# Kernel optimization log

Measured on AMD Instinct MI355X. Metric: run time of the kernel, lower is better.

The kernel has to match this reference:

```python
import jax, jax.numpy as jnp
import numpy as np

EPS = 1e-5
DN = ('NCHW', 'OIHW', 'NCHW')


def _conv(x, w, b, stride, pad):
    y = jax.lax.conv_general_dilated(x, w, (stride, stride), [(pad, pad), (pad, pad)], dimension_numbers=DN)
    return y + b[None, :, None, None]


def _conv_t(x, w, b, stride, pad):
    # ConvTranspose2d(w: [in, out, k, k]) == conv with flipped/transposed kernel + lhs dilation
    k = w.shape[2]
    wt = jnp.flip(w, (2, 3)).transpose(1, 0, 2, 3)
    p = k - 1 - pad
    y = jax.lax.conv_general_dilated(x, wt, (1, 1), [(p, p), (p, p)], lhs_dilation=(stride, stride), dimension_numbers=DN)
    return y + b[None, :, None, None]


def _bn(x, g, b):
    # training-mode BatchNorm2d: biased batch stats over (N, H, W)
    m = x.mean((0, 2, 3), keepdims=True)
    v = x.var((0, 2, 3), keepdims=True)
    return (x - m) * jax.lax.rsqrt(v + EPS) * g[None, :, None, None] + b[None, :, None, None]


def _forward(args):
    (x, ec1_w, ec1_b, ebn1_g, ebn1_b, ec2_w, ec2_b, ebn2_g, ebn2_b,
     er1_w, er1_b, ebnr1_g, ebnr1_b, er2_w, er2_b, ebnr2_g, ebnr2_b,
     eproj_w, eproj_b, emb,
     dproj_w, dproj_b, dr1_w, dr1_b, dbn1_g, dbn1_b, dr2_w, dr2_b, dbn2_g, dbn2_b,
     dt1_w, dt1_b, dbn3_g, dbn3_b, dt2_w, dt2_b) = args
    relu = jax.nn.relu
    sg = jax.lax.stop_gradient
    # ---- encoder ----
    h = relu(_bn(_conv(x, ec1_w, ec1_b, 2, 1), ebn1_g, ebn1_b))
    h = relu(_bn(_conv(h, ec2_w, ec2_b, 2, 1), ebn2_g, ebn2_b))
    h = h + relu(_bn(_conv(h, er1_w, er1_b, 1, 1), ebnr1_g, ebnr1_b))
    h = h + relu(_bn(_conv(h, er2_w, er2_b, 1, 0), ebnr2_g, ebnr2_b))
    enc = _conv(h, eproj_w, eproj_b, 1, 0)  # [B, D, H, W]
    B, C, H, W = enc.shape
    # torch .view(B, -1, C): raw row-major reshape (no permute) -- reproduced exactly
    qi = enc.reshape(B, -1, C)  # [B, H*W, D]
    # squared euclidean distances; argmin identical to torch.cdist argmin
    d2 = (qi * qi).sum(-1, keepdims=True) - 2.0 * jnp.einsum('bnd,kd->bnk', qi, emb) + (emb * emb).sum(-1)
    closest = jnp.argmin(d2, axis=-1)  # [B, H*W]
    quantized = emb[closest]           # [B, H*W, D]
    commitment = jnp.mean((sg(quantized) - qi) ** 2)
    codebook = jnp.mean((quantized - sg(qi)) ** 2)
    quantize_loss = codebook + 0.25 * commitment
    # straight-through estimator
    quant_out = (qi + sg(quantized - qi)).reshape(B, C, H, W)
    # ---- decoder ----
    h = _conv(quant_out, dproj_w, dproj_b, 1, 0)
    h = h + relu(_bn(_conv(h, dr1_w, dr1_b, 1, 1), dbn1_g, dbn1_b))
    h = h + relu(_bn(_conv(h, dr2_w, dr2_b, 1, 1), dbn2_g, dbn2_b))
    h = relu(_bn(_conv_t(h, dt1_w, dt1_b, 2, 1), dbn3_g, dbn3_b))
    out = _conv_t(h, dt2_w, dt2_b, 2, 1)
    return out, closest, quantize_loss


def setup_inputs() -> dict:
    key = jax.random.key(0)
    ks = iter(jax.random.split(key, 32))
    def nrm(shape, fan):
        return jax.random.normal(next(ks), shape, jnp.float32) / np.float32(np.sqrt(fan))
    B, CH, S = 8, 3, 256
    K, D, HID, RES = 512, 64, 256, 128
    z = jnp.zeros
    o = jnp.ones
    return {
        'x': jax.random.normal(next(ks), (B, CH, S, S), jnp.float32),
        'ec1_w': nrm((HID, CH, 4, 4), CH * 16), 'ec1_b': z((HID,)),
        'ebn1_g': o((HID,)), 'ebn1_b': z((HID,)),
        'ec2_w': nrm((RES, HID, 4, 4), HID * 16), 'ec2_b': z((RES,)),
        'ebn2_g': o((RES,)), 'ebn2_b': z((RES,)),
        'er1_w': nrm((RES, RES, 3, 3), RES * 9), 'er1_b': z((RES,)),
        'ebnr1_g': o((RES,)), 'ebnr1_b': z((RES,)),
        'er2_w': nrm((RES, RES, 1, 1), RES), 'er2_b': z((RES,)),
        'ebnr2_g': o((RES,)), 'ebnr2_b': z((RES,)),
        'eproj_w': nrm((D, RES, 1, 1), RES), 'eproj_b': z((D,)),
        'emb': jax.random.normal(next(ks), (K, D), jnp.float32),
        'dproj_w': nrm((RES, D, 1, 1), D), 'dproj_b': z((RES,)),
        'dr1_w': nrm((RES, RES, 3, 3), RES * 9), 'dr1_b': z((RES,)),
        'dbn1_g': o((RES,)), 'dbn1_b': z((RES,)),
        'dr2_w': nrm((RES, RES, 3, 3), RES * 9), 'dr2_b': z((RES,)),
        'dbn2_g': o((RES,)), 'dbn2_b': z((RES,)),
        'dt1_w': nrm((RES, HID, 4, 4), RES * 16), 'dt1_b': z((HID,)),
        'dbn3_g': o((HID,)), 'dbn3_b': z((HID,)),
        'dt2_w': nrm((HID, CH, 4, 4), HID * 16), 'dt2_b': z((CH,)),
    }


def reference(x, ec1_w, ec1_b, ebn1_g, ebn1_b, ec2_w, ec2_b, ebn2_g, ebn2_b,
              er1_w, er1_b, ebnr1_g, ebnr1_b, er2_w, er2_b, ebnr2_g, ebnr2_b,
              eproj_w, eproj_b, emb,
              dproj_w, dproj_b, dr1_w, dr1_b, dbn1_g, dbn1_b, dr2_w, dr2_b, dbn2_g, dbn2_b,
              dt1_w, dt1_b, dbn3_g, dbn3_b, dt2_w, dt2_b):
    return _forward((x, ec1_w, ec1_b, ebn1_g, ebn1_b, ec2_w, ec2_b, ebn2_g, ebn2_b,
                     er1_w, er1_b, ebnr1_g, ebnr1_b, er2_w, er2_b, ebnr2_g, ebnr2_b,
                     eproj_w, eproj_b, emb,
                     dproj_w, dproj_b, dr1_w, dr1_b, dbn1_g, dbn1_b, dr2_w, dr2_b, dbn2_g, dbn2_b,
                     dt1_w, dt1_b, dbn3_g, dbn3_b, dt2_w, dt2_b))
```

## Files before the change

kernel.cpp:

```cpp
#include <hip/hip_runtime.h>
#include <hip/hip_bf16.h>

typedef unsigned short u16;
typedef unsigned int u32;

static __device__ __forceinline__ float b2f(u16 u) { return __uint_as_float(((u32)u) << 16); }
static __device__ __forceinline__ float draw(const void* p, size_t i, int fl) {
  return fl ? b2f(((const u16*)p)[i]) : ((const float*)p)[i];
}

#define KC 16
#define TP 128
#define TC 64

__global__ void detect_k(const u32* g, int* flag) {
  if (threadIdx.x == 0) flag[0] = (g[0] == 0x3F800000u) ? 0 : 1;
}

template<int KSQ, int MODE, int RAW, int BNIN>
__global__ __launch_bounds__(256) void gemm_conv(
    const void* __restrict__ Xv, const float* __restrict__ Wt, const float* __restrict__ bias,
    float* __restrict__ Y, int Cin, int Co, int Hin, int Win, int HWo, int wshift,
    int stride, int pad, int Ktot, size_t xoff, const int* __restrict__ dflag,
    const float* __restrict__ bnc,
    const float* __restrict__ q2v, const float* __restrict__ emb2,
    float2* __restrict__ vqout, int nct)
{
  __shared__ float As[KC][TP];
  __shared__ float Bs[KC][TC];
  int fl = 0;
  if constexpr (RAW) fl = dflag[0];
  const int tid = threadIdx.x;
  const int tx = tid & 15, ty = tid >> 4;
  const int p0 = blockIdx.x * TP;
  const int c0 = blockIdx.y * TC;
  int b, py, px;
  if constexpr (MODE == 1) { b = blockIdx.z >> 2; py = (blockIdx.z >> 1) & 1; px = blockIdx.z & 1; }
  else { b = blockIdx.z; py = 0; px = 0; }
  const int Wout = 1 << wshift;
  const size_t xbase = (size_t)b * Cin * Hin * Win + xoff;
  const float* Wb = (MODE == 1) ? (Wt + (size_t)(py * 2 + px) * Ktot * Co) : Wt;
  float acc[8][4];
#pragma unroll
  for (int i = 0; i < 8; ++i)
#pragma unroll
    for (int j = 0; j < 4; ++j) acc[i][j] = 0.f;

  for (int kb = 0; kb < Ktot; kb += KC) {
#pragma unroll
    for (int i = 0; i < 8; ++i) {
      int e = tid + i * 256;
      int kk = e >> 7, p = e & 127;
      int k = kb + kk;
      float v = 0.f;
      if constexpr (MODE == 2) {
        v = ((const float*)Xv)[(size_t)(p0 + p) * 64 + k];
      } else {
        int pg = p0 + p;
        int ho = pg >> wshift, wo = pg & (Wout - 1);
        int ci, hi, wi;
        if constexpr (MODE == 0) {
          ci = k / KSQ;
          int r = k - ci * KSQ;
          int kh, kw;
          if (KSQ == 16) { kh = r >> 2; kw = r & 3; }
          else if (KSQ == 9) { kh = r / 3; kw = r - kh * 3; }
          else { kh = 0; kw = 0; }
          hi = ho * stride - pad + kh;
          wi = wo * stride - pad + kw;
        } else {
          ci = k >> 2;
          int a = (k >> 1) & 1, b2 = k & 1;
          hi = ho + py - a;
          wi = wo + px - b2;
        }
        if ((unsigned)hi < (unsigned)Hin && (unsigned)wi < (unsigned)Win) {
          size_t xi = xbase + ((size_t)ci * Hin + hi) * Win + wi;
          if constexpr (RAW) v = draw(Xv, xi, fl);
          else v = ((const float*)Xv)[xi];
          if constexpr (BNIN) v = fmaxf(fmaf(v, bnc[ci], bnc[Cin + ci]), 0.f);
        }
      }
      As[kk][p] = v;
    }
    {
      int e0 = tid * 4;
      int kk = e0 >> 6, c = e0 & 63;
      *(float4*)&Bs[kk][c] = *(const float4*)&Wb[(size_t)(kb + kk) * Co + c0 + c];
    }
    __syncthreads();
#pragma unroll
    for (int kk = 0; kk < KC; ++kk) {
      float a0[8], b0[4];
      *(float4*)&a0[0] = *(const float4*)&As[kk][tx * 4];
      *(float4*)&a0[4] = *(const float4*)&As[kk][64 + tx * 4];
      *(float4*)&b0[0] = *(const float4*)&Bs[kk][ty * 4];
#pragma unroll
      for (int i = 0; i < 8; ++i)
#pragma unroll
        for (int j = 0; j < 4; ++j)
          acc[i][j] = fmaf(a0[i], b0[j], acc[i][j]);
    }
    __syncthreads();
  }

  if constexpr (MODE == 0) {
#pragma unroll
    for (int j = 0; j < 4; ++j) {
      int c = c0 + ty * 4 + j;
      float bv = bias ? bias[c] : 0.f;
      float* dst = Y + ((size_t)b * Co + c) * (size_t)HWo;
      float4 v0 = make_float4(acc[0][j] + bv, acc[1][j] + bv, acc[2][j] + bv, acc[3][j] + bv);
      float4 v1 = make_float4(acc[4][j] + bv, acc[5][j] + bv, acc[6][j] + bv, acc[7][j] + bv);
      *(float4*)&dst[p0 + tx * 4] = v0;
      *(float4*)&dst[p0 + 64 + tx * 4] = v1;
    }
  } else if constexpr (MODE == 1) {
#pragma unroll
    for (int j = 0; j < 4; ++j) {
      int c = c0 + ty * 4 + j;
      float bv = bias ? bias[c] : 0.f;
      float* dst = Y + ((size_t)b * Co + c) * (size_t)(HWo * 4);
#pragma unroll
      for (int i = 0; i < 8; ++i) {
        int pp = (i < 4) ? (tx * 4 + i) : (64 + tx * 4 + (i - 4));
        int pg = p0 + pp;
        int hp = pg >> wshift, wp = pg & (Wout - 1);
        dst[(2 * hp + py) * (Wout * 2) + (2 * wp + px)] = acc[i][j] + bv;
      }
    }
  } else {
    __shared__ float mvv[TP][17];
    __shared__ int   mii[TP][17];
#pragma unroll
    for (int i = 0; i < 8; ++i) {
      int pp = (i < 4) ? (tx * 4 + i) : (64 + tx * 4 + (i - 4));
      float q2t = q2v[p0 + pp];
      float best = 3.4e38f; int bi = 0;
#pragma unroll
      for (int j = 0; j < 4; ++j) {
        int c = c0 + ty * 4 + j;
        float d = q2t - 2.f * acc[i][j] + emb2[c];
        if (d < best) { best = d; bi = c; }
      }
      mvv[pp][ty] = best; mii[pp][ty] = bi;
    }
    __syncthreads();
    if (tid < TP) {
      float best = 3.4e38f; int bi = 0;
#pragma unroll
      for (int t = 0; t < 16; ++t) {
        float v = mvv[tid][t];
        if (v < best) { best = v; bi = mii[tid][t]; }
      }
      vqout[(size_t)(p0 + tid) * nct + blockIdx.y] = make_float2(best, __int_as_float(bi));
    }
  }
}

__global__ void wt_conv_k(const void* __restrict__ w, float* __restrict__ wt, int Co, int Kt,
                          const int* __restrict__ flag) {
  int fl = flag[0];
  int i = blockIdx.x * 256 + threadIdx.x;
  if (i >= Kt * Co) return;
  int k = i / Co, c = i - k * Co;
  wt[i] = draw(w, (size_t)c * Kt + k, fl);
}

__global__ void wt_convt_k(const void* __restrict__ w, float* __restrict__ wt, int Cin, int Co,
                           const int* __restrict__ flag) {
  int fl = flag[0];
  int total = 4 * Cin * 4 * Co;
  int i = blockIdx.x * 256 + threadIdx.x;
  if (i >= total) return;
  int c = i % Co;
  int t = i / Co;
  int k = t % (Cin * 4);
  int ph = t / (Cin * 4);
  int ci = k >> 2; int a = (k >> 1) & 1; int b2 = k & 1;
  int py = ph >> 1, px = ph & 1;
  int kh = py ? (a ? 2 : 0) : (a ? 3 : 1);
  int kw = px ? (b2 ? 2 : 0) : (b2 ? 3 : 1);
  wt[i] = draw(w, (((size_t)ci * Co + c) * 4 + kh) * 4 + kw, fl);
}

__global__ void copy_k(const void* __restrict__ src, float* __restrict__ dst, int n,
                       const int* __restrict__ flag) {
  int fl = flag[0];
  int i = blockIdx.x * 256 + threadIdx.x;
  if (i < n) dst[i] = draw(src, i, fl);
}

__global__ void prep_emb(const void* __restrict__ emb, float* __restrict__ embT,
                         float* __restrict__ emb2, const int* __restrict__ flag) {
  int fl = flag[0];
  int i = blockIdx.x * 256 + threadIdx.x;
  if (i < 64 * 512) {
    int d = i >> 9, k = i & 511;
    embT[i] = draw(emb, (size_t)k * 64 + d, fl);
  }
  if (i < 512) {
    float s = 0.f;
    for (int d = 0; d < 64; ++d) { float v = draw(emb, (size_t)i * 64 + d, fl); s = fmaf(v, v, s); }
    emb2[i] = s;
  }
}

__global__ void prep_small(const void* a0, const void* a1, const void* a2, const void* a3,
                           const void* a4, const void* a5, const void* a6, const void* a7,
                           const void* a8, const void* a9, const void* a10, const void* a11,
                           const void* a12, const void* a13, const void* a14, const void* a15,
                           const void* a16, float* __restrict__ dst, const int* __restrict__ flag)
{
  int fl = flag[0];
  const void* srcs[17] = {a0,a1,a2,a3,a4,a5,a6,a7,a8,a9,a10,a11,a12,a13,a14,a15,a16};
  const int offs[18] = {0,256,512,640,768,896,1024,1152,1280,1408,1536,1664,1792,2048,2304,2368,2496,2499};
  for (int s = 0; s < 17; ++s) {
    int n = offs[s + 1] - offs[s];
    for (int i = threadIdx.x; i < n; i += 256)
      dst[offs[s] + i] = draw(srcs[s], i, fl);
  }
}

__global__ __launch_bounds__(256) void bn_stats(const float* __restrict__ x, float* __restrict__ part,
                                                int C, int hwshift, int cpb, int NBtot, int blkoff)
{
  int c = blockIdx.x, blk = blockIdx.y;
  int HW = 1 << hwshift;
  float s = 0.f, s2 = 0.f;
  size_t base = (size_t)blk * cpb;
  int n4 = cpb >> 2;
  for (int i = threadIdx.x; i < n4; i += 256) {
    size_t e = base + ((size_t)i << 2);
    int bb = (int)(e >> hwshift);
    int r = (int)(e & (HW - 1));
    float4 v = *(const float4*)&x[(((size_t)bb * C + c) << hwshift) + r];
    s += (v.x + v.y) + (v.z + v.w);
    s2 += (v.x * v.x + v.y * v.y) + (v.z * v.z + v.w * v.w);
  }
  __shared__ float sa[256], sb[256];
  sa[threadIdx.x] = s; sb[threadIdx.x] = s2;
  __syncthreads();
  for (int o = 128; o; o >>= 1) {
    if (threadIdx.x < o) { sa[threadIdx.x] += sa[threadIdx.x + o]; sb[threadIdx.x] += sb[threadIdx.x + o]; }
    __syncthreads();
  }
  if (threadIdx.x == 0) {
    part[((size_t)c * NBtot + blkoff + blk) * 2] = sa[0];
    part[((size_t)c * NBtot + blkoff + blk) * 2 + 1] = sb[0];
  }
}

__global__ void bn_final(const float* __restrict__ part, int NB, const float* __restrict__ g,
                         const float* __restrict__ bt, float* __restrict__ coef, int C, float invn)
{
  int c = threadIdx.x;
  if (c >= C) return;
  float s = 0.f, s2 = 0.f;
  for (int j = 0; j < NB; ++j) { s += part[((size_t)c * NB + j) * 2]; s2 += part[((size_t)c * NB + j) * 2 + 1]; }
  float m = s * invn;
  float var = fmaxf(s2 * invn - m * m, 0.f);
  float A = g[c] / sqrtf(var + 1e-5f);
  coef[c] = A;
  coef[C + c] = bt[c] - m * A;
}

__global__ __launch_bounds__(256) void bn_apply(float* __restrict__ dst, const float* __restrict__ xr,
                                                const float* __restrict__ res, const float* __restrict__ coef,
                                                int C, int hwshift, size_t n4)
{
  size_t i = (size_t)blockIdx.x * 256 + threadIdx.x;
  if (i >= n4) return;
  size_t e = i << 2;
  int c = (int)((e >> hwshift) & (C - 1));
  float A = coef[c], Bv = coef[C + c];
  float4 x = *(const float4*)(xr + e);
  float4 o;
  o.x = fmaxf(fmaf(x.x, A, Bv), 0.f);
  o.y = fmaxf(fmaf(x.y, A, Bv), 0.f);
  o.z = fmaxf(fmaf(x.z, A, Bv), 0.f);
  o.w = fmaxf(fmaf(x.w, A, Bv), 0.f);
  if (res) { float4 r = *(const float4*)(res + e); o.x += r.x; o.y += r.y; o.z += r.z; o.w += r.w; }
  *(float4*)(dst + e) = o;
}

__global__ void q2_k(const float* __restrict__ q, float* __restrict__ q2, int ntok) {
  int t = blockIdx.x * 256 + threadIdx.x;
  if (t >= ntok) return;
  const float* p = q + (size_t)t * 64;
  float s = 0.f;
  for (int d = 0; d < 64; ++d) s = fmaf(p[d], p[d], s);
  q2[t] = s;
}

__global__ void vq_final(const float2* __restrict__ vqp, int nct, int* __restrict__ closest,
                         float* __restrict__ outc, int ntok)
{
  int t = blockIdx.x * 256 + threadIdx.x;
  if (t >= ntok) return;
  float best = 3.4e38f; int bi = 0;
  for (int j = 0; j < nct; ++j) {
    float2 v = vqp[(size_t)t * nct + j];
    if (v.x < best) { best = v.x; bi = __float_as_int(v.y); }
  }
  closest[t] = bi;
  outc[t] = (float)bi;
}

__global__ __launch_bounds__(256) void quant_loss(float* __restrict__ qc, const int* __restrict__ closest,
                                                  const float* __restrict__ embT, float* __restrict__ lpart)
{
  int wid = threadIdx.x >> 6;
  int lane = threadIdx.x & 63;
  int tok = blockIdx.x * 4 + wid;
  int idx = closest[tok];
  float e = embT[(size_t)lane * 512 + idx];
  size_t qoff = (size_t)tok * 64 + lane;
  float q = qc[qoff];
  float d = e - q;
  float s = d * d;
  for (int o = 32; o; o >>= 1) s += __shfl_down(s, o);
  qc[qoff] = e;
  __shared__ float sm[4];
  if (lane == 0) sm[wid] = s;
  __syncthreads();
  if (threadIdx.x == 0) lpart[blockIdx.x] = (sm[0] + sm[1]) + (sm[2] + sm[3]);
}

__global__ __launch_bounds__(256) void loss_final(const float* __restrict__ lpart, float* __restrict__ o)
{
  __shared__ float sm[256];
  float s = 0.f;
  int base = threadIdx.x * 32;
  for (int i = 0; i < 32; ++i) s += lpart[base + i];
  sm[threadIdx.x] = s;
  __syncthreads();
  for (int t = 128; t; t >>= 1) { if (threadIdx.x < t) sm[threadIdx.x] += sm[threadIdx.x + t]; __syncthreads(); }
  if (threadIdx.x == 0) o[0] = sm[0] * (1.25f / 2097152.f);
}

__global__ __launch_bounds__(256) void convt_small(const float* __restrict__ Xall, const float* __restrict__ wf,
                                                   const float* __restrict__ coef,
                                                   const float* __restrict__ bias3, float* __restrict__ Y)
{
  __shared__ float wl[12288];
  __shared__ float cA[256], cB[256];
  for (int i = threadIdx.x; i < 12288; i += 256) wl[i] = wf[i];
  for (int i = threadIdx.x; i < 256; i += 256) { cA[i] = coef[i]; cB[i] = coef[256 + i]; }
  __syncthreads();
  int b = blockIdx.x >> 8;
  int ho = blockIdx.x & 255;
  const float* X = Xall + (size_t)b * 4194304;
  int half = threadIdx.x >> 7;
  int wop = threadIdx.x & 127;
  int wo = wop * 2 + half;
  float a0 = 0.f, a1 = 0.f, a2 = 0.f;
  for (int kh = 0; kh < 4; ++kh) {
    int h2 = ho + 1 - kh;
    if (h2 & 1) continue;
    int hi = h2 >> 1;
    if ((unsigned)hi >= 128u) continue;
    for (int kw = half ? 0 : 1; kw < 4; kw += 2) {
      int w2 = wo + 1 - kw;
      int wi = w2 >> 1;
      if (w2 < 0 || (unsigned)wi >= 128u) continue;
      const float* xp = X + (size_t)hi * 128 + wi;
      const float* wp = wl + kh * 4 + kw;
      for (int ci = 0; ci < 256; ++ci) {
        float raw = xp[(size_t)ci * 16384];
        float xv = fmaxf(fmaf(raw, cA[ci], cB[ci]), 0.f);
        a0 = fmaf(xv, wp[ci * 48], a0);
        a1 = fmaf(xv, wp[ci * 48 + 16], a1);
        a2 = fmaf(xv, wp[ci * 48 + 32], a2);
      }
    }
  }
  size_t o = (size_t)b * 196608 + (size_t)ho * 256 + wo;
  Y[o]          = a0 + bias3[0];
  Y[o + 65536]  = a1 + bias3[1];
  Y[o + 131072] = a2 + bias3[2];
}

extern "C" void kernel_launch(void* const* d_in, const int* in_sizes, int n_in,
                              void* d_out, int out_size, void* d_ws, size_t ws_size,
                              hipStream_t stream)
{
  (void)in_sizes; (void)n_in; (void)out_size; (void)ws_size;
  float* out = (float*)d_out;

  float* ws = (float*)d_ws;
  size_t off = 0;
  auto alloc = [&](size_t n) { float* p = ws + off; off += (n + 255) & ~(size_t)255; return p; };
  float* big    = alloc(33554432);
  float* Abuf   = alloc(4194304);
  float* Bbuf   = alloc(4194304);
  float* Cbuf   = alloc(2097152);
  float* wt_ec1 = alloc(48 * 256);
  float* wt_ec2 = alloc(4096 * 128);
  float* wt_er1 = alloc(1152 * 128);
  float* wt_er2 = alloc(128 * 128);
  float* wt_epj = alloc(128 * 64);
  float* wt_dpj = alloc(64 * 128);
  float* wt_dr1 = alloc(1152 * 128);
  float* wt_dr2 = alloc(1152 * 128);
  float* wt_dt1 = alloc(4 * 512 * 256);
  float* wt_dt2 = alloc(12288);
  float* embT   = alloc(64 * 512);
  float* emb2   = alloc(512);
  float* q2buf  = alloc(32768);
  float* bnpart = alloc(256 * 32 * 2);
  float* bncoef = alloc(512);
  float* smallp = alloc(4096);
  float2* vqp   = (float2*)alloc(32768 * 8 * 2);
  int*   closest = (int*)alloc(32768);
  float* lpart  = alloc(8192);
  int*   dflag  = (int*)alloc(64);

  detect_k<<<1, 64, 0, stream>>>((const u32*)d_in[3], dflag);

  wt_conv_k<<<(48 * 256 + 255) / 256, 256, 0, stream>>>(d_in[1], wt_ec1, 256, 48, dflag);
  wt_conv_k<<<(4096 * 128 + 255) / 256, 256, 0, stream>>>(d_in[5], wt_ec2, 128, 4096, dflag);
  wt_conv_k<<<(1152 * 128 + 255) / 256, 256, 0, stream>>>(d_in[9], wt_er1, 128, 1152, dflag);
  wt_conv_k<<<(128 * 128 + 255) / 256, 256, 0, stream>>>(d_in[13], wt_er2, 128, 128, dflag);
  wt_conv_k<<<(128 * 64 + 255) / 256, 256, 0, stream>>>(d_in[17], wt_epj, 64, 128, dflag);
  wt_conv_k<<<(64 * 128 + 255) / 256, 256, 0, stream>>>(d_in[20], wt_dpj, 128, 64, dflag);
  wt_conv_k<<<(1152 * 128 + 255) / 256, 256, 0, stream>>>(d_in[22], wt_dr1, 128, 1152, dflag);
  wt_conv_k<<<(1152 * 128 + 255) / 256, 256, 0, stream>>>(d_in[26], wt_dr2, 128, 1152, dflag);
  wt_convt_k<<<(4 * 512 * 256 + 255) / 256, 256, 0, stream>>>(d_in[30], wt_dt1, 128, 256, dflag);
  copy_k<<<48, 256, 0, stream>>>(d_in[34], wt_dt2, 12288, dflag);
  prep_emb<<<128, 256, 0, stream>>>(d_in[19], embT, emb2, dflag);
  prep_small<<<1, 256, 0, stream>>>(
      d_in[3], d_in[4], d_in[7], d_in[8], d_in[11], d_in[12], d_in[15], d_in[16],
      d_in[24], d_in[25], d_in[28], d_in[29], d_in[32], d_in[33],
      d_in[18], d_in[21], d_in[35], smallp, dflag);

  gemm_conv<16, 0, 1, 0><<<dim3(128, 4, 8), 256, 0, stream>>>(d_in[0], wt_ec1, nullptr, big,
      3, 256, 256, 256, 16384, 7, 2, 1, 48, 0, dflag, nullptr, nullptr, nullptr, nullptr, 0);
  bn_stats<<<dim3(256, 32), 256, 0, stream>>>(big, bnpart, 256, 14, 4096, 32, 0);
  bn_final<<<1, 256, 0, stream>>>(bnpart, 32, smallp + 0, smallp + 256, bncoef, 256, 1.f / 131072.f);
  gemm_conv<16, 0, 0, 1><<<dim3(32, 2, 8), 256, 0, stream>>>(big, wt_ec2, nullptr, Abuf,
      256, 128, 128, 128, 4096, 6, 2, 1, 4096, 0, dflag, bncoef, nullptr, nullptr, nullptr, 0);
  bn_stats<<<dim3(128, 32), 256, 0, stream>>>(Abuf, bnpart, 128, 12, 1024, 32, 0);
  bn_final<<<1, 256, 0, stream>>>(bnpart, 32, smallp + 512, smallp + 640, bncoef, 128, 1.f / 32768.f);
  bn_apply<<<4096, 256, 0, stream>>>(Abuf, Abuf, nullptr, bncoef, 128, 12, 1048576);
  gemm_conv<9, 0, 0, 0><<<dim3(32, 2, 8), 256, 0, stream>>>(Abuf, wt_er1, nullptr, Bbuf,
      128, 128, 64, 64, 4096, 6, 1, 1, 1152, 0, dflag, nullptr, nullptr, nullptr, nullptr, 0);
  bn_stats<<<dim3(128, 32), 256, 0, stream>>>(Bbuf, bnpart, 128, 12, 1024, 32, 0);
  bn_final<<<1, 256, 0, stream>>>(bnpart, 32, smallp + 768, smallp + 896, bncoef, 128, 1.f / 32768.f);
  bn_apply<<<4096, 256, 0, stream>>>(Bbuf, Bbuf, Abuf, bncoef, 128, 12, 1048576);
  gemm_conv<1, 0, 0, 0><<<dim3(32, 2, 8), 256, 0, stream>>>(Bbuf, wt_er2, nullptr, Abuf,
      128, 128, 64, 64, 4096, 6, 1, 0, 128, 0, dflag, nullptr, nullptr, nullptr, nullptr, 0);
  bn_stats<<<dim3(128, 32), 256, 0, stream>>>(Abuf, bnpart, 128, 12, 1024, 32, 0);
  bn_final<<<1, 256, 0, stream>>>(bnpart, 32, smallp + 1024, smallp + 1152, bncoef, 128, 1.f / 32768.f);
  bn_apply<<<4096, 256, 0, stream>>>(Abuf, Abuf, Bbuf, bncoef, 128, 12, 1048576);
  gemm_conv<1, 0, 0, 0><<<dim3(32, 1, 8), 256, 0, stream>>>(Abuf, wt_epj, smallp + 2304, Cbuf,
      128, 64, 64, 64, 4096, 6, 1, 0, 128, 0, dflag, nullptr, nullptr, nullptr, nullptr, 0);

  q2_k<<<128, 256, 0, stream>>>(Cbuf, q2buf, 32768);
  gemm_conv<1, 2, 0, 0><<<dim3(256, 8, 1), 256, 0, stream>>>(Cbuf, embT, nullptr, nullptr,
      1, 512, 1, 1, 32768, 0, 0, 0, 64, 0, dflag, nullptr, q2buf, emb2, vqp, 8);
  vq_final<<<128, 256, 0, stream>>>(vqp, 8, closest, out + 1572864, 32768);
  quant_loss<<<8192, 256, 0, stream>>>(Cbuf, closest, embT, lpart);
  loss_final<<<1, 256, 0, stream>>>(lpart, out + 1605632);

  gemm_conv<1, 0, 0, 0><<<dim3(32, 2, 8), 256, 0, stream>>>(Cbuf, wt_dpj, smallp + 2368, Abuf,
      64, 128, 64, 64, 4096, 6, 1, 0, 64, 0, dflag, nullptr, nullptr, nullptr, nullptr, 0);
  gemm_conv<9, 0, 0, 0><<<dim3(32, 2, 8), 256, 0, stream>>>(Abuf, wt_dr1, nullptr, Bbuf,
      128, 128, 64, 64, 4096, 6, 1, 1, 1152, 0, dflag, nullptr, nullptr, nullptr, nullptr, 0);
  bn_stats<<<dim3(128, 32), 256, 0, stream>>>(Bbuf, bnpart, 128, 12, 1024, 32, 0);
  bn_final<<<1, 256, 0, stream>>>(bnpart, 32, smallp + 1280, smallp + 1408, bncoef, 128, 1.f / 32768.f);
  bn_apply<<<4096, 256, 0, stream>>>(Bbuf, Bbuf, Abuf, bncoef, 128, 12, 1048576);
  gemm_conv<9, 0, 0, 0><<<dim3(32, 2, 8), 256, 0, stream>>>(Bbuf, wt_dr2, nullptr, Abuf,
      128, 128, 64, 64, 4096, 6, 1, 1, 1152, 0, dflag, nullptr, nullptr, nullptr, nullptr, 0);
  bn_stats<<<dim3(128, 32), 256, 0, stream>>>(Abuf, bnpart, 128, 12, 1024, 32, 0);
  bn_final<<<1, 256, 0, stream>>>(bnpart, 32, smallp + 1536, smallp + 1664, bncoef, 128, 1.f / 32768.f);
  bn_apply<<<4096, 256, 0, stream>>>(Abuf, Abuf, Bbuf, bncoef, 128, 12, 1048576);
  gemm_conv<16, 1, 0, 0><<<dim3(32, 4, 32), 256, 0, stream>>>(Abuf, wt_dt1, nullptr, big,
      128, 256, 64, 64, 4096, 6, 0, 0, 512, 0, dflag, nullptr, nullptr, nullptr, nullptr, 0);
  bn_stats<<<dim3(256, 32), 256, 0, stream>>>(big, bnpart, 256, 14, 4096, 32, 0);
  bn_final<<<1, 256, 0, stream>>>(bnpart, 32, smallp + 1792, smallp + 2048, bncoef, 256, 1.f / 131072.f);
  convt_small<<<2048, 256, 0, stream>>>(big, wt_dt2, bncoef, smallp + 2496, out);
}
```

Before: 2.588 ms.

## Run decoder convolutions on bf16 MFMA matrix cores instead of FP32 FMA GEMM

Adds an mfma_conv kernel that stages bf16 weight and im2col tiles in XOR-swizzled shared memory and computes with 16x16x32 bf16 MFMA instructions. The decoder projection, both decoder 3x3 residual convs and the first transposed conv use it, with weights pre-cast to bf16 (the transposed-conv weights are rearranged per output phase). The goal is to move the main decoder FLOPs from scalar FP32 FMAs onto matrix cores. In exchange, activations and weights are rounded to bf16, which lowers precision, and the now-unused transposed-conv mode is removed from the FP32 GEMM.

```diff
diff --git a/kernel.cpp b/kernel.cpp
--- a/kernel.cpp
+++ b/kernel.cpp
@@ -4,7 +4,14 @@
 typedef unsigned short u16;
 typedef unsigned int u32;
 
+typedef short bfrag __attribute__((ext_vector_type(8)));
+typedef float f32x4 __attribute__((ext_vector_type(4)));
+
 static __device__ __forceinline__ float b2f(u16 u) { return __uint_as_float(((u32)u) << 16); }
+static __device__ __forceinline__ u16 f2b(float f) {
+  u32 u = __float_as_uint(f);
+  return (u16)((u + (((u >> 16) & 1u) + 0x7fffu)) >> 16);
+}
 static __device__ __forceinline__ float draw(const void* p, size_t i, int fl) {
   return fl ? b2f(((const u16*)p)[i]) : ((const float*)p)[i];
 }
@@ -34,12 +41,10 @@
   const int tx = tid & 15, ty = tid >> 4;
   const int p0 = blockIdx.x * TP;
   const int c0 = blockIdx.y * TC;
-  int b, py, px;
-  if constexpr (MODE == 1) { b = blockIdx.z >> 2; py = (blockIdx.z >> 1) & 1; px = blockIdx.z & 1; }
-  else { b = blockIdx.z; py = 0; px = 0; }
+  int b = blockIdx.z;
   const int Wout = 1 << wshift;
   const size_t xbase = (size_t)b * Cin * Hin * Win + xoff;
-  const float* Wb = (MODE == 1) ? (Wt + (size_t)(py * 2 + px) * Ktot * Co) : Wt;
+  const float* Wb = Wt;
   float acc[8][4];
 #pragma unroll
   for (int i = 0; i < 8; ++i)
@@ -58,22 +63,14 @@
       } else {
         int pg = p0 + p;
         int ho = pg >> wshift, wo = pg & (Wout - 1);
-        int ci, hi, wi;
-        if constexpr (MODE == 0) {
-          ci = k / KSQ;
-          int r = k - ci * KSQ;
-          int kh, kw;
-          if (KSQ == 16) { kh = r >> 2; kw = r & 3; }
-          else if (KSQ == 9) { kh = r / 3; kw = r - kh * 3; }
-          else { kh = 0; kw = 0; }
-          hi = ho * stride - pad + kh;
-          wi = wo * stride - pad + kw;
-        } else {
-          ci = k >> 2;
-          int a = (k >> 1) & 1, b2 = k & 1;
-          hi = ho + py - a;
-          wi = wo + px - b2;
-        }
+        int ci = k / KSQ;
+        int r = k - ci * KSQ;
+        int kh, kw;
+        if (KSQ == 16) { kh = r >> 2; kw = r & 3; }
+        else if (KSQ == 9) { kh = r / 3; kw = r - kh * 3; }
+        else { kh = 0; kw = 0; }
+        int hi = ho * stride - pad + kh;
+        int wi = wo * stride - pad + kw;
         if ((unsigned)hi < (unsigned)Hin && (unsigned)wi < (unsigned)Win) {
           size_t xi = xbase + ((size_t)ci * Hin + hi) * Win + wi;
           if constexpr (RAW) v = draw(Xv, xi, fl);
@@ -115,20 +112,6 @@
       *(float4*)&dst[p0 + tx * 4] = v0;
       *(float4*)&dst[p0 + 64 + tx * 4] = v1;
     }
-  } else if constexpr (MODE == 1) {
-#pragma unroll
-    for (int j = 0; j < 4; ++j) {
-      int c = c0 + ty * 4 + j;
-      float bv = bias ? bias[c] : 0.f;
-      float* dst = Y + ((size_t)b * Co + c) * (size_t)(HWo * 4);
-#pragma unroll
-      for (int i = 0; i < 8; ++i) {
-        int pp = (i < 4) ? (tx * 4 + i) : (64 + tx * 4 + (i - 4));
-        int pg = p0 + pp;
-        int hp = pg >> wshift, wp = pg & (Wout - 1);
-        dst[(2 * hp + py) * (Wout * 2) + (2 * wp + px)] = acc[i][j] + bv;
-      }
-    }
   } else {
     __shared__ float mvv[TP][17];
     __shared__ int   mii[TP][17];
@@ -154,6 +137,114 @@
         if (v < best) { best = v; bi = mii[tid][t]; }
       }
       vqout[(size_t)(p0 + tid) * nct + blockIdx.y] = make_float2(best, __int_as_float(bi));
+    }
+  }
+}
+
+template<int KSQ, int MODE, int COT>
+__global__ __launch_bounds__(256) void mfma_conv(
+    const float* __restrict__ X, const u16* __restrict__ Wbf, const float* __restrict__ bias,
+    float* __restrict__ Y, int Cin, int Co, int Hin, int Win, int wshift,
+    int stride, int pad, int Ktot)
+{
+  constexpr int MR = COT / 32;
+  __shared__ u16 Al[COT * 32];
+  __shared__ u16 Bl[128 * 32];
+  const int tid = threadIdx.x;
+  const int lane = tid & 63, wave = tid >> 6;
+  const int wr = wave >> 1, wc = wave & 1;
+  const int p0 = blockIdx.x * 128;
+  const int c0 = blockIdx.y * COT;
+  int b, py, px;
+  if constexpr (MODE == 1) { b = blockIdx.z >> 2; py = (blockIdx.z >> 1) & 1; px = blockIdx.z & 1; }
+  else { b = blockIdx.z; py = 0; px = 0; }
+  const int Wout = 1 << wshift;
+  const float* Xb = X + (size_t)b * Cin * Hin * Win;
+  const u16* Wb = Wbf + (MODE == 1 ? (size_t)(py * 2 + px) * Co * Ktot : 0);
+
+  f32x4 acc[MR][4];
+#pragma unroll
+  for (int m = 0; m < MR; ++m)
+#pragma unroll
+    for (int n = 0; n < 4; ++n) acc[m][n] = f32x4{0.f, 0.f, 0.f, 0.f};
+
+  for (int kb = 0; kb < Ktot; kb += 32) {
+#pragma unroll
+    for (int rr = 0; rr < COT / 64; ++rr) {
+      int idx = rr * 256 + tid;
+      int co = idx >> 2, ch = idx & 3;
+      uint4 v = *(const uint4*)&Wb[(size_t)(c0 + co) * Ktot + kb + ch * 8];
+      *(uint4*)&Al[co * 32 + ((ch ^ (co & 3)) << 3)] = v;
+    }
+#pragma unroll
+    for (int i = 0; i < 16; ++i) {
+      int e = i * 256 + tid;
+      int kk = e >> 7, p = e & 127;
+      int k = kb + kk;
+      u16 v = 0;
+      int pg = p0 + p;
+      int ho = pg >> wshift, wo = pg & (Wout - 1);
+      int ci, hi, wi;
+      if constexpr (MODE == 0) {
+        ci = k / KSQ;
+        int r2 = k - ci * KSQ;
+        int kh, kw;
+        if (KSQ == 9) { kh = r2 / 3; kw = r2 - kh * 3; }
+        else { kh = 0; kw = 0; }
+        hi = ho * stride - pad + kh;
+        wi = wo * stride - pad + kw;
+      } else {
+        ci = k >> 2;
+        int a = (k >> 1) & 1, b2 = k & 1;
+        hi = ho + py - a;
+        wi = wo + px - b2;
+      }
+      if ((unsigned)hi < (unsigned)Hin && (unsigned)wi < (unsigned)Win)
+        v = f2b(Xb[((size_t)ci * Hin + hi) * Win + wi]);
+      Bl[p * 32 + (((kk >> 3) ^ (p & 3)) << 3) + (kk & 7)] = v;
+    }
+    __syncthreads();
+    bfrag af[MR], bv[4];
+#pragma unroll
+    for (int m = 0; m < MR; ++m) {
+      int co = wr * (COT / 2) + m * 16 + (lane & 15);
+      af[m] = *(const bfrag*)&Al[co * 32 + (((lane >> 4) ^ (co & 3)) << 3)];
+    }
+#pragma unroll
+    for (int n = 0; n < 4; ++n) {
+      int p = wc * 64 + n * 16 + (lane & 15);
+      bv[n] = *(const bfrag*)&Bl[p * 32 + (((lane >> 4) ^ (p & 3)) << 3)];
+    }
+#pragma unroll
+    for (int m = 0; m < MR; ++m)
+#pragma unroll
+      for (int n = 0; n < 4; ++n)
+        acc[m][n] = __builtin_amdgcn_mfma_f32_16x16x32_bf16(af[m], bv[n], acc[m][n], 0, 0, 0);
+    __syncthreads();
+  }
+
+#pragma unroll
+  for (int m = 0; m < MR; ++m) {
+#pragma unroll
+    for (int r = 0; r < 4; ++r) {
+      int co = c0 + wr * (COT / 2) + m * 16 + ((lane >> 4) << 2) + r;
+      float bvs = bias ? bias[co] : 0.f;
+      if constexpr (MODE == 0) {
+        float* dst = Y + ((size_t)b * Co + co) * (size_t)(Hin * Win);
+#pragma unroll
+        for (int n = 0; n < 4; ++n) {
+          int pix = p0 + wc * 64 + n * 16 + (lane & 15);
+          dst[pix] = acc[m][n][r] + bvs;
+        }
+      } else {
+        float* dst = Y + ((size_t)b * Co + co) * (size_t)(Hin * Win * 4);
+#pragma unroll
+        for (int n = 0; n < 4; ++n) {
+          int pix = p0 + wc * 64 + n * 16 + (lane & 15);
+          int hp = pix >> wshift, wp = pix & (Wout - 1);
+          dst[(2 * hp + py) * (2 * Wout) + 2 * wp + px] = acc[m][n][r] + bvs;
+        }
+      }
     }
   }
 }
@@ -167,21 +258,26 @@
   wt[i] = draw(w, (size_t)c * Kt + k, fl);
 }
 
-__global__ void wt_convt_k(const void* __restrict__ w, float* __restrict__ wt, int Cin, int Co,
+__global__ void cast_bf16_k(const void* __restrict__ src, u16* __restrict__ dst, int n,
+                            const int* __restrict__ flag) {
+  int fl = flag[0];
+  int i = blockIdx.x * 256 + threadIdx.x;
+  if (i < n) dst[i] = f2b(draw(src, i, fl));
+}
+
+__global__ void wt_dt1bf_k(const void* __restrict__ w, u16* __restrict__ dst,
                            const int* __restrict__ flag) {
   int fl = flag[0];
-  int total = 4 * Cin * 4 * Co;
   int i = blockIdx.x * 256 + threadIdx.x;
-  if (i >= total) return;
-  int c = i % Co;
-  int t = i / Co;
-  int k = t % (Cin * 4);
-  int ph = t / (Cin * 4);
-  int ci = k >> 2; int a = (k >> 1) & 1; int b2 = k & 1;
+  if (i >= 4 * 256 * 512) return;
+  int k = i & 511;
+  int co = (i >> 9) & 255;
+  int ph = i >> 17;
+  int ci = k >> 2, a = (k >> 1) & 1, b2 = k & 1;
   int py = ph >> 1, px = ph & 1;
   int kh = py ? (a ? 2 : 0) : (a ? 3 : 1);
   int kw = px ? (b2 ? 2 : 0) : (b2 ? 3 : 1);
-  wt[i] = draw(w, (((size_t)ci * Co + c) * 4 + kh) * 4 + kw, fl);
+  dst[i] = f2b(draw(w, (((size_t)ci * 256 + co) * 4 + kh) * 4 + kw, fl));
 }
 
 __global__ void copy_k(const void* __restrict__ src, float* __restrict__ dst, int n,
@@ -400,11 +496,11 @@
   float* wt_er1 = alloc(1152 * 128);
   float* wt_er2 = alloc(128 * 128);
   float* wt_epj = alloc(128 * 64);
-  float* wt_dpj = alloc(64 * 128);
-  float* wt_dr1 = alloc(1152 * 128);
-  float* wt_dr2 = alloc(1152 * 128);
-  float* wt_dt1 = alloc(4 * 512 * 256);
   float* wt_dt2 = alloc(12288);
+  u16*  wbf_dpj = (u16*)alloc(4096);
+  u16*  wbf_dr1 = (u16*)alloc(73728);
+  u16*  wbf_dr2 = (u16*)alloc(73728);
+  u16*  wbf_dt1 = (u16*)alloc(262144);
   float* embT   = alloc(64 * 512);
   float* emb2   = alloc(512);
   float* q2buf  = alloc(32768);
@@ -423,10 +519,10 @@
   wt_conv_k<<<(1152 * 128 + 255) / 256, 256, 0, stream>>>(d_in[9], wt_er1, 128, 1152, dflag);
   wt_conv_k<<<(128 * 128 + 255) / 256, 256, 0, stream>>>(d_in[13], wt_er2, 128, 128, dflag);
   wt_conv_k<<<(128 * 64 + 255) / 256, 256, 0, stream>>>(d_in[17], wt_epj, 64, 128, dflag);
-  wt_conv_k<<<(64 * 128 + 255) / 256, 256, 0, stream>>>(d_in[20], wt_dpj, 128, 64, dflag);
-  wt_conv_k<<<(1152 * 128 + 255) / 256, 256, 0, stream>>>(d_in[22], wt_dr1, 128, 1152, dflag);
-  wt_conv_k<<<(1152 * 128 + 255) / 256, 256, 0, stream>>>(d_in[26], wt_dr2, 128, 1152, dflag);
-  wt_convt_k<<<(4 * 512 * 256 + 255) / 256, 256, 0, stream>>>(d_in[30], wt_dt1, 128, 256, dflag);
+  cast_bf16_k<<<32, 256, 0, stream>>>(d_in[20], wbf_dpj, 8192, dflag);
+  cast_bf16_k<<<576, 256, 0, stream>>>(d_in[22], wbf_dr1, 147456, dflag);
+  cast_bf16_k<<<576, 256, 0, stream>>>(d_in[26], wbf_dr2, 147456, dflag);
+  wt_dt1bf_k<<<2048, 256, 0, stream>>>(d_in[30], wbf_dt1, dflag);
   copy_k<<<48, 256, 0, stream>>>(d_in[34], wt_dt2, 12288, dflag);
   prep_emb<<<128, 256, 0, stream>>>(d_in[19], embT, emb2, dflag);
   prep_small<<<1, 256, 0, stream>>>(
@@ -463,20 +559,20 @@
   quant_loss<<<8192, 256, 0, stream>>>(Cbuf, closest, embT, lpart);
   loss_final<<<1, 256, 0, stream>>>(lpart, out + 1605632);
 
-  gemm_conv<1, 0, 0, 0><<<dim3(32, 2, 8), 256, 0, stream>>>(Cbuf, wt_dpj, smallp + 2368, Abuf,
-      64, 128, 64, 64, 4096, 6, 1, 0, 64, 0, dflag, nullptr, nullptr, nullptr, nullptr, 0);
-  gemm_conv<9, 0, 0, 0><<<dim3(32, 2, 8), 256, 0, stream>>>(Abuf, wt_dr1, nullptr, Bbuf,
-      128, 128, 64, 64, 4096, 6, 1, 1, 1152, 0, dflag, nullptr, nullptr, nullptr, nullptr, 0);
+  mfma_conv<1, 0, 64><<<dim3(32, 2, 8), 256, 0, stream>>>(Cbuf, wbf_dpj, smallp + 2368, Abuf,
+      64, 128, 64, 64, 6, 1, 0, 64);
+  mfma_conv<9, 0, 64><<<dim3(32, 2, 8), 256, 0, stream>>>(Abuf, wbf_dr1, nullptr, Bbuf,
+      128, 128, 64, 64, 6, 1, 1, 1152);
   bn_stats<<<dim3(128, 32), 256, 0, stream>>>(Bbuf, bnpart, 128, 12, 1024, 32, 0);
   bn_final<<<1, 256, 0, stream>>>(bnpart, 32, smallp + 1280, smallp + 1408, bncoef, 128, 1.f / 32768.f);
   bn_apply<<<4096, 256, 0, stream>>>(Bbuf, Bbuf, Abuf, bncoef, 128, 12, 1048576);
-  gemm_conv<9, 0, 0, 0><<<dim3(32, 2, 8), 256, 0, stream>>>(Bbuf, wt_dr2, nullptr, Abuf,
-      128, 128, 64, 64, 4096, 6, 1, 1, 1152, 0, dflag, nullptr, nullptr, nullptr, nullptr, 0);
+  mfma_conv<9, 0, 64><<<dim3(32, 2, 8), 256, 0, stream>>>(Bbuf, wbf_dr2, nullptr, Abuf,
+      128, 128, 64, 64, 6, 1, 1, 1152);
   bn_stats<<<dim3(128, 32), 256, 0, stream>>>(Abuf, bnpart, 128, 12, 1024, 32, 0);
   bn_final<<<1, 256, 0, stream>>>(bnpart, 32, smallp + 1536, smallp + 1664, bncoef, 128, 1.f / 32768.f);
   bn_apply<<<4096, 256, 0, stream>>>(Abuf, Abuf, Bbuf, bncoef, 128, 12, 1048576);
-  gemm_conv<16, 1, 0, 0><<<dim3(32, 4, 32), 256, 0, stream>>>(Abuf, wt_dt1, nullptr, big,
-      128, 256, 64, 64, 4096, 6, 0, 0, 512, 0, dflag, nullptr, nullptr, nullptr, nullptr, 0);
+  mfma_conv<16, 1, 128><<<dim3(32, 2, 32), 256, 0, stream>>>(Abuf, wbf_dt1, nullptr, big,
+      128, 256, 64, 64, 6, 0, 0, 512);
   bn_stats<<<dim3(256, 32), 256, 0, stream>>>(big, bnpart, 256, 14, 4096, 32, 0);
   bn_final<<<1, 256, 0, stream>>>(bnpart, 32, smallp + 1792, smallp + 2048, bncoef, 256, 1.f / 131072.f);
   convt_small<<<2048, 256, 0, stream>>>(big, wt_dt2, bncoef, smallp + 2496, out);
```

New measurement: 2.276 ms. 1.14x faster.
